# Kernel tuning notes

Measured on AMD Instinct MI355X. Metric: run time of the kernel, lower is better.

Reference implementation:

```python
import jax, jax.numpy as jnp
import numpy as np

N_NODES = 100000
N_EDGES = 1600000
IN_C = 128
HID_C = 16
HEADS = 4
OUT_C = 32
NEG_SLOPE = 0.2


def _gat_conv(x, src, dst, W, a_src, a_dst, b, heads, C):
    """One PyG-style GATConv (v1) with self-loops already appended to src/dst."""
    N = x.shape[0]
    h = (x @ W).reshape(N, heads, C)                      # [N,H,C]
    al_src = jnp.einsum('nhc,hc->nh', h, a_src)           # [N,H]
    al_dst = jnp.einsum('nhc,hc->nh', h, a_dst)           # [N,H]
    e = jax.nn.leaky_relu(al_src[src] + al_dst[dst], NEG_SLOPE)  # [E,H]
    # segment softmax over destination nodes (numerically stable)
    m = jax.ops.segment_max(e, dst, num_segments=N)       # [N,H]
    m = jnp.where(jnp.isfinite(m), m, 0.0)
    ee = jnp.exp(e - m[dst])
    denom = jax.ops.segment_sum(ee, dst, num_segments=N)  # [N,H]
    alpha = ee / denom[dst]                               # [E,H]
    out = jax.ops.segment_sum(h[src] * alpha[:, :, None], dst, num_segments=N)  # [N,H,C]
    return out.reshape(N, heads * C) + b


def setup_inputs() -> dict:
    key = jax.random.key(0)
    ks = jax.random.split(key, 16)
    s = 0.05
    x = jax.random.normal(ks[0], (N_NODES, IN_C), dtype=jnp.float32)
    edge_index = jax.random.randint(ks[1], (2, N_EDGES), 0, N_NODES, dtype=jnp.int64)
    d = {
        'x': x,
        'edge_index': edge_index,
        'W1': jax.random.normal(ks[2], (IN_C, HEADS * HID_C), dtype=jnp.float32) * s,
        'a_src1': jax.random.normal(ks[3], (HEADS, HID_C), dtype=jnp.float32) * s,
        'a_dst1': jax.random.normal(ks[4], (HEADS, HID_C), dtype=jnp.float32) * s,
        'b1': jnp.zeros((HEADS * HID_C,), dtype=jnp.float32),
        'W2': jax.random.normal(ks[5], (HEADS * HID_C, HEADS * HID_C), dtype=jnp.float32) * s,
        'a_src2': jax.random.normal(ks[6], (HEADS, HID_C), dtype=jnp.float32) * s,
        'a_dst2': jax.random.normal(ks[7], (HEADS, HID_C), dtype=jnp.float32) * s,
        'b2': jnp.zeros((HEADS * HID_C,), dtype=jnp.float32),
        'W3': jax.random.normal(ks[8], (HEADS * HID_C, OUT_C), dtype=jnp.float32) * s,
        'a_src3': jax.random.normal(ks[9], (1, OUT_C), dtype=jnp.float32) * s,
        'a_dst3': jax.random.normal(ks[10], (1, OUT_C), dtype=jnp.float32) * s,
        'b3': jnp.zeros((OUT_C,), dtype=jnp.float32),
    }
    return d


def reference(x, edge_index, W1, a_src1, a_dst1, b1, W2, a_src2, a_dst2, b2,
              W3, a_src3, a_dst3, b3):
    N = x.shape[0]
    loop = jnp.arange(N, dtype=edge_index.dtype)
    src = jnp.concatenate([edge_index[0], loop])  # PyG add_self_loops=True
    dst = jnp.concatenate([edge_index[1], loop])
    h = jax.nn.relu(_gat_conv(x, src, dst, W1, a_src1, a_dst1, b1, HEADS, HID_C))
    # dropout p=0.5 is identity in eval mode
    h = jax.nn.relu(_gat_conv(h, src, dst, W2, a_src2, a_dst2, b2, HEADS, HID_C))
    out = _gat_conv(h, src, dst, W3, a_src3, a_dst3, b3, 1, OUT_C)  # [N, OUT_C]
    return out  # .squeeze(-2) is a no-op on [N, OUT_C] with N>1
```

## Files before the change

### kernel.cpp

```cpp
#include <hip/hip_runtime.h>
#include <hip/hip_fp16.h>

#define N_NODES 100000
#define N_EDGES 1600000
#define NPART   8
#define PART_SZ (N_NODES / NPART)
#define CAP 48
#define BSH  10
#define NBIN 98
#define SCAP2 4096
#define SSH2 12
#define EPB  2048

static __device__ __forceinline__ float lrelu(float z) { return z > 0.f ? z : 0.2f * z; }
static __device__ __forceinline__ int imin(int a, int b) { return a < b ? a : b; }

static __device__ __forceinline__ unsigned pack2h(float a, float b) {
    return __builtin_bit_cast(unsigned, __floats2half2_rn(a, b));
}

__global__ __launch_bounds__(256) void bucket_build(const int* __restrict__ ei, int* __restrict__ tails,
                                                    unsigned* __restrict__ stage) {
    __shared__ int lcnt[NBIN];
    __shared__ int lbase[NBIN];
    int tid = threadIdx.x;
    if (tid < NBIN) lcnt[tid] = 0;
    __syncthreads();

    int stripe = blockIdx.x & 7;
    int e0 = blockIdx.x * EPB;
    int binv[EPB / 256];
    int slotv[EPB / 256];
    unsigned vv[EPB / 256];
#pragma unroll
    for (int k = 0; k < EPB / 256; ++k) {
        int t = e0 + k * 256 + tid;
        binv[k] = -1;
        if (t < N_EDGES) {
            int d = __builtin_nontemporal_load(ei + N_EDGES + t);
            int s = __builtin_nontemporal_load(ei + t);
            int b = d >> BSH;
            vv[k] = ((unsigned)(d & ((1 << BSH) - 1)) << 17) | (unsigned)s;
            slotv[k] = atomicAdd(&lcnt[b], 1);
            binv[k] = b;
        }
    }
    __syncthreads();

    if (tid < NBIN) lbase[tid] = atomicAdd(&tails[stripe * 128 + tid], lcnt[tid]);
    __syncthreads();

#pragma unroll
    for (int k = 0; k < EPB / 256; ++k) {
        if (binv[k] >= 0) {
            int pos = lbase[binv[k]] + slotv[k];
            if (pos < SCAP2)
                stage[((((unsigned)binv[k] << 3) | (unsigned)stripe) << SSH2) + (unsigned)pos] = vv[k];
        }
    }
}

__global__ __launch_bounds__(1024) void bucket_fill(const int* __restrict__ tails, const unsigned* __restrict__ stage,
                                                    int* __restrict__ cnt, int* __restrict__ srcs) {
    __shared__ int lc[1 << BSH];
    int tid = threadIdx.x;
    int bin = blockIdx.x;
    int base = bin << BSH;
    int nn = N_NODES - base; if (nn > (1 << BSH)) nn = 1 << BSH;
    if (tid < nn) {
        lc[tid] = 1;
        srcs[(base + tid) * CAP] = base + tid;
    }
    __syncthreads();

    for (int st = 0; st < 8; ++st) {
        int len = tails[st * 128 + bin];
        if (len > SCAP2) len = SCAP2;
        const unsigned* sl = stage + ((((unsigned)bin << 3) | (unsigned)st) << SSH2);
        for (int i = tid; i < len; i += 1024) {
            unsigned v = __builtin_nontemporal_load(sl + i);
            int dloc = (int)(v >> 17);
            int s = (int)(v & 0x1FFFFu);
            int slot = atomicAdd(&lc[dloc], 1);
            if (slot < CAP) srcs[(base + dloc) * CAP + slot] = s;
        }
    }
    __syncthreads();
    if (tid < nn) cnt[base + tid] = lc[tid];
}

template <int IN, int OUT, int HEADS, int NPB>
__global__ __launch_bounds__(256) void gemm_al(const float* __restrict__ x, const float* __restrict__ W,
                                               const float* __restrict__ asrc, const float* __restrict__ adst,
                                               unsigned short* __restrict__ h, float* __restrict__ als,
                                               float* __restrict__ ald) {
    constexpr int SPLIT = OUT / 16;
    constexpr int STRIDE = IN + 1;
    constexpr int F4PT = NPB * (IN / 4) / 256;
    constexpr int KCH = (IN * OUT * 4 > 16384) ? (IN / 2) : IN;
    __shared__ float sx[NPB * STRIDE];
    __shared__ float sw[KCH * OUT];
    int t = threadIdx.x;
    long base = (long)blockIdx.x * NPB;

#pragma unroll
    for (int p = 0; p < F4PT; ++p) {
        int e = p * 256 + t;
        int row = e / (IN / 4);
        int c4 = e % (IN / 4);
        long gr = base + row;
        if (gr >= N_NODES) gr = N_NODES - 1;
        float4 v = *reinterpret_cast<const float4*>(&x[gr * IN + c4 * 4]);
        float* d = &sx[row * STRIDE + c4 * 4];
        d[0] = v.x; d[1] = v.y; d[2] = v.z; d[3] = v.w;
    }

    int w = t >> 6, lane = t & 63;
    int s = __builtin_amdgcn_readfirstlane(w % SPLIT);
    int grp = __builtin_amdgcn_readfirstlane(w / SPLIT);
    int r = grp * 64 + lane;
    long n = base + r;

    float acc[16];
#pragma unroll
    for (int j = 0; j < 16; ++j) acc[j] = 0.f;

    for (int k0 = 0; k0 < IN; k0 += KCH) {
        __syncthreads();
#pragma unroll
        for (int e = t; e < KCH * OUT / 4; e += 256)
            reinterpret_cast<float4*>(sw)[e] =
                reinterpret_cast<const float4*>(W + (long)k0 * OUT)[e];
        __syncthreads();

        const float* swb = sw + s * 16;
#pragma unroll 8
        for (int k = 0; k < KCH; ++k) {
            float xv = sx[r * STRIDE + k0 + k];
            const float* Wr = swb + k * OUT;
#pragma unroll
            for (int j = 0; j < 16; ++j) acc[j] = fmaf(xv, Wr[j], acc[j]);
        }
    }

    if (n < N_NODES) {
        unsigned u[8];
#pragma unroll
        for (int k = 0; k < 8; ++k)
            u[k] = pack2h(acc[2 * k], acc[2 * k + 1]);
        uint4* dst = reinterpret_cast<uint4*>(&h[n * OUT + s * 16]);
        dst[0] = make_uint4(u[0], u[1], u[2], u[3]);
        dst[1] = make_uint4(u[4], u[5], u[6], u[7]);
    }

    float ps = 0.f, pd = 0.f;
#pragma unroll
    for (int j = 0; j < 16; ++j) {
        ps = fmaf(acc[j], asrc[s * 16 + j], ps);
        pd = fmaf(acc[j], adst[s * 16 + j], pd);
    }
    if (HEADS == SPLIT) {
        if (n < N_NODES) {
            als[n * HEADS + s] = ps;
            ald[n * HEADS + s] = pd;
        }
    } else {
        __syncthreads();
        sx[r * 2 + s] = ps;
        sx[NPB * 2 + r * 2 + s] = pd;
        __syncthreads();
        if (t < NPB) {
            long nn = base + t;
            if (nn < N_NODES) {
                als[nn] = sx[t * 2] + sx[t * 2 + 1];
                ald[nn] = sx[NPB * 2 + t * 2] + sx[NPB * 2 + t * 2 + 1];
            }
        }
    }
}

static __device__ __forceinline__ int agg_node(int blk, int wid) {
    return (blk & 7) * PART_SZ + (blk >> 3) * 4 + wid;
}

__global__ __launch_bounds__(256, 8) void agg_h4(const int* __restrict__ cnt, const int* __restrict__ srcs,
                                                 const unsigned short* __restrict__ h, const float* __restrict__ als,
                                                 const float* __restrict__ ald, const float* __restrict__ bias,
                                                 float* __restrict__ g, int do_relu) {
    const uint4* hrow = reinterpret_cast<const uint4*>(h);
    int wid = threadIdx.x >> 6, lane = threadIdx.x & 63;
    int n = agg_node(blockIdx.x, wid);
    if (n >= N_NODES) return;
    int q = lane >> 3, cc = lane & 7;
    int hd = cc >> 1;
    float ad = ald[n * 4 + hd];
    int deg = cnt[n]; if (deg > CAP) deg = CAP;
    int dm1 = deg - 1;
    int sl = srcs[n * CAP + imin(lane, dm1)];

    int s0 = __shfl(sl, imin(0 * 8 + q, dm1));
    int s1 = __shfl(sl, imin(1 * 8 + q, dm1));
    int s2 = __shfl(sl, imin(2 * 8 + q, dm1));
    int s3 = __shfl(sl, imin(3 * 8 + q, dm1));
    float al0 = als[s0 * 4 + hd];
    float al1 = als[s1 * 4 + hd];
    float al2 = als[s2 * 4 + hd];
    float al3 = als[s3 * 4 + hd];
    uint4 hv0 = hrow[(long)s0 * 8 + cc];
    uint4 hv1 = hrow[(long)s1 * 8 + cc];
    uint4 hv2 = hrow[(long)s2 * 8 + cc];
    uint4 hv3 = hrow[(long)s3 * 8 + cc];
    __builtin_amdgcn_sched_barrier(0);

    float a0 = 0.f, a1 = 0.f, a2 = 0.f, a3 = 0.f, a4 = 0.f, a5 = 0.f, a6 = 0.f, a7 = 0.f;
    float den = 0.f;
#define ACCUM(AL, HV, T)                                                \
    {                                                                   \
        float w = ((T) * 8 + q) < deg ? __expf(lrelu((AL) + ad)) : 0.f; \
        den += w;                                                       \
        __half2 p0 = __builtin_bit_cast(__half2, (HV).x);               \
        __half2 p1 = __builtin_bit_cast(__half2, (HV).y);               \
        __half2 p2 = __builtin_bit_cast(__half2, (HV).z);               \
        __half2 p3 = __builtin_bit_cast(__half2, (HV).w);               \
        a0 = fmaf(w, (float)p0.x, a0); a1 = fmaf(w, (float)p0.y, a1);   \
        a2 = fmaf(w, (float)p1.x, a2); a3 = fmaf(w, (float)p1.y, a3);   \
        a4 = fmaf(w, (float)p2.x, a4); a5 = fmaf(w, (float)p2.y, a5);   \
        a6 = fmaf(w, (float)p3.x, a6); a7 = fmaf(w, (float)p3.y, a7);   \
    }
    ACCUM(al0, hv0, 0)
    ACCUM(al1, hv1, 1)
    ACCUM(al2, hv2, 2)
    ACCUM(al3, hv3, 3)

    if (__builtin_expect(deg > 32, 0)) {
        for (int e = 32; e < deg; e += 8) {
            int ee = e + q;
            int s = __shfl(sl, imin(ee, dm1));
            float al = als[s * 4 + hd];
            uint4 hv = hrow[(long)s * 8 + cc];
            float w = ee < deg ? __expf(lrelu(al + ad)) : 0.f;
            den += w;
            __half2 p0 = __builtin_bit_cast(__half2, hv.x);
            __half2 p1 = __builtin_bit_cast(__half2, hv.y);
            __half2 p2 = __builtin_bit_cast(__half2, hv.z);
            __half2 p3 = __builtin_bit_cast(__half2, hv.w);
            a0 = fmaf(w, (float)p0.x, a0); a1 = fmaf(w, (float)p0.y, a1);
            a2 = fmaf(w, (float)p1.x, a2); a3 = fmaf(w, (float)p1.y, a3);
            a4 = fmaf(w, (float)p2.x, a4); a5 = fmaf(w, (float)p2.y, a5);
            a6 = fmaf(w, (float)p3.x, a6); a7 = fmaf(w, (float)p3.y, a7);
        }
    }
#undef ACCUM

#pragma unroll
    for (int d = 8; d <= 32; d <<= 1) {
        a0 += __shfl_xor(a0, d); a1 += __shfl_xor(a1, d);
        a2 += __shfl_xor(a2, d); a3 += __shfl_xor(a3, d);
        a4 += __shfl_xor(a4, d); a5 += __shfl_xor(a5, d);
        a6 += __shfl_xor(a6, d); a7 += __shfl_xor(a7, d);
        den += __shfl_xor(den, d);
    }
    if (q == 0) {
        float4 b0 = *reinterpret_cast<const float4*>(&bias[cc * 8]);
        float4 b1 = *reinterpret_cast<const float4*>(&bias[cc * 8 + 4]);
        float inv = 1.f / den;
        float4 o0, o1;
        o0.x = fmaf(a0, inv, b0.x); o0.y = fmaf(a1, inv, b0.y);
        o0.z = fmaf(a2, inv, b0.z); o0.w = fmaf(a3, inv, b0.w);
        o1.x = fmaf(a4, inv, b1.x); o1.y = fmaf(a5, inv, b1.y);
        o1.z = fmaf(a6, inv, b1.z); o1.w = fmaf(a7, inv, b1.w);
        if (do_relu) {
            o0.x = fmaxf(o0.x, 0.f); o0.y = fmaxf(o0.y, 0.f);
            o0.z = fmaxf(o0.z, 0.f); o0.w = fmaxf(o0.w, 0.f);
            o1.x = fmaxf(o1.x, 0.f); o1.y = fmaxf(o1.y, 0.f);
            o1.z = fmaxf(o1.z, 0.f); o1.w = fmaxf(o1.w, 0.f);
        }
        *reinterpret_cast<float4*>(&g[(long)n * 64 + cc * 8]) = o0;
        *reinterpret_cast<float4*>(&g[(long)n * 64 + cc * 8 + 4]) = o1;
    }
}

__global__ __launch_bounds__(256, 8) void agg_h1(const int* __restrict__ cnt, const int* __restrict__ srcs,
                                                 const unsigned short* __restrict__ h3, const float* __restrict__ als,
                                                 const float* __restrict__ ald, const float* __restrict__ bias,
                                                 float* __restrict__ out) {
    const uint4* hrow = reinterpret_cast<const uint4*>(h3);
    int wid = threadIdx.x >> 6, lane = threadIdx.x & 63;
    int n = agg_node(blockIdx.x, wid);
    if (n >= N_NODES) return;
    int q = lane >> 2, cc = lane & 3;
    float ad = ald[n];
    int deg = cnt[n]; if (deg > CAP) deg = CAP;
    int dm1 = deg - 1;
    int sl = srcs[n * CAP + imin(lane, dm1)];

    int s0 = __shfl(sl, imin(0 * 16 + q, dm1));
    int s1 = __shfl(sl, imin(1 * 16 + q, dm1));
    float al0 = als[s0];
    float al1 = als[s1];
    uint4 hv0 = hrow[(long)s0 * 4 + cc];
    uint4 hv1 = hrow[(long)s1 * 4 + cc];
    __builtin_amdgcn_sched_barrier(0);

    float a0 = 0.f, a1 = 0.f, a2 = 0.f, a3 = 0.f, a4 = 0.f, a5 = 0.f, a6 = 0.f, a7 = 0.f;
    float den = 0.f;
#define ACCUM1(AL, HV, T)                                                \
    {                                                                    \
        float w = ((T) * 16 + q) < deg ? __expf(lrelu((AL) + ad)) : 0.f; \
        den += w;                                                        \
        __half2 p0 = __builtin_bit_cast(__half2, (HV).x);                \
        __half2 p1 = __builtin_bit_cast(__half2, (HV).y);                \
        __half2 p2 = __builtin_bit_cast(__half2, (HV).z);                \
        __half2 p3 = __builtin_bit_cast(__half2, (HV).w);                \
        a0 = fmaf(w, (float)p0.x, a0); a1 = fmaf(w, (float)p0.y, a1);    \
        a2 = fmaf(w, (float)p1.x, a2); a3 = fmaf(w, (float)p1.y, a3);    \
        a4 = fmaf(w, (float)p2.x, a4); a5 = fmaf(w, (float)p2.y, a5);    \
        a6 = fmaf(w, (float)p3.x, a6); a7 = fmaf(w, (float)p3.y, a7);    \
    }
    ACCUM1(al0, hv0, 0)
    ACCUM1(al1, hv1, 1)

    if (__builtin_expect(deg > 32, 0)) {
        for (int e = 32; e < deg; e += 16) {
            int ee = e + q;
            int s = __shfl(sl, imin(ee, dm1));
            float al = als[s];
            uint4 hv = hrow[(long)s * 4 + cc];
            float w = ee < deg ? __expf(lrelu(al + ad)) : 0.f;
            den += w;
            __half2 p0 = __builtin_bit_cast(__half2, hv.x);
            __half2 p1 = __builtin_bit_cast(__half2, hv.y);
            __half2 p2 = __builtin_bit_cast(__half2, hv.z);
            __half2 p3 = __builtin_bit_cast(__half2, hv.w);
            a0 = fmaf(w, (float)p0.x, a0); a1 = fmaf(w, (float)p0.y, a1);
            a2 = fmaf(w, (float)p1.x, a2); a3 = fmaf(w, (float)p1.y, a3);
            a4 = fmaf(w, (float)p2.x, a4); a5 = fmaf(w, (float)p2.y, a5);
            a6 = fmaf(w, (float)p3.x, a6); a7 = fmaf(w, (float)p3.y, a7);
        }
    }
#undef ACCUM1

#pragma unroll
    for (int d = 4; d <= 32; d <<= 1) {
        a0 += __shfl_xor(a0, d); a1 += __shfl_xor(a1, d);
        a2 += __shfl_xor(a2, d); a3 += __shfl_xor(a3, d);
        a4 += __shfl_xor(a4, d); a5 += __shfl_xor(a5, d);
        a6 += __shfl_xor(a6, d); a7 += __shfl_xor(a7, d);
        den += __shfl_xor(den, d);
    }
    if (q == 0) {
        float4 b0 = *reinterpret_cast<const float4*>(&bias[cc * 8]);
        float4 b1 = *reinterpret_cast<const float4*>(&bias[cc * 8 + 4]);
        float inv = 1.f / den;
        float4 o0, o1;
        o0.x = fmaf(a0, inv, b0.x); o0.y = fmaf(a1, inv, b0.y);
        o0.z = fmaf(a2, inv, b0.z); o0.w = fmaf(a3, inv, b0.w);
        o1.x = fmaf(a4, inv, b1.x); o1.y = fmaf(a5, inv, b1.y);
        o1.z = fmaf(a6, inv, b1.z); o1.w = fmaf(a7, inv, b1.w);
        *reinterpret_cast<float4*>(&out[(long)n * 32 + cc * 8]) = o0;
        *reinterpret_cast<float4*>(&out[(long)n * 32 + cc * 8 + 4]) = o1;
    }
}

extern "C" void kernel_launch(void* const* d_in, const int* in_sizes, int n_in,
                              void* d_out, int out_size, void* d_ws, size_t ws_size,
                              hipStream_t stream) {
    (void)in_sizes; (void)n_in; (void)out_size; (void)ws_size;
    const float* x   = (const float*)d_in[0];
    const int*   ei  = (const int*)d_in[1];
    const float* W1  = (const float*)d_in[2];
    const float* as1 = (const float*)d_in[3];
    const float* ad1 = (const float*)d_in[4];
    const float* b1  = (const float*)d_in[5];
    const float* W2  = (const float*)d_in[6];
    const float* as2 = (const float*)d_in[7];
    const float* ad2 = (const float*)d_in[8];
    const float* b2  = (const float*)d_in[9];
    const float* W3  = (const float*)d_in[10];
    const float* as3 = (const float*)d_in[11];
    const float* ad3 = (const float*)d_in[12];
    const float* b3  = (const float*)d_in[13];
    float* out = (float*)d_out;

    char* w = (char*)d_ws;
    auto alloc = [&](size_t bytes) {
        void* p = (void*)w;
        w += (bytes + 255) & ~(size_t)255;
        return p;
    };
    int*            cnt   = (int*)alloc((size_t)N_NODES * 4);
    int*            tails = (int*)alloc((size_t)1024 * 4);
    int*            srcs  = (int*)alloc((size_t)N_NODES * CAP * 4);
    unsigned short* h     = (unsigned short*)alloc((size_t)N_NODES * 64 * 2);
    float*          g     = (float*)alloc((size_t)N_NODES * 64 * 4);
    float*          als   = (float*)alloc((size_t)N_NODES * 4 * 4);
    float*          ald   = (float*)alloc((size_t)N_NODES * 4 * 4);
    unsigned*       stage = (unsigned*)g;

    hipMemsetAsync(tails, 0, (size_t)1024 * 4, stream);

    int g64  = (N_NODES + 63) / 64;
    int g128 = (N_NODES + 127) / 128;
    int gAgg = ((N_NODES + 3) / 4 + 7) & ~7;
    int gBuild = (N_EDGES + EPB - 1) / EPB;

    bucket_build<<<gBuild, 256, 0, stream>>>(ei, tails, stage);
    bucket_fill<<<NBIN, 1024, 0, stream>>>(tails, stage, cnt, srcs);

    gemm_al<128, 64, 4, 64><<<g64, 256, 0, stream>>>(x, W1, as1, ad1, h, als, ald);
    agg_h4<<<gAgg, 256, 0, stream>>>(cnt, srcs, h, als, ald, b1, g, 1);
    gemm_al<64, 64, 4, 64><<<g64, 256, 0, stream>>>(g, W2, as2, ad2, h, als, ald);
    agg_h4<<<gAgg, 256, 0, stream>>>(cnt, srcs, h, als, ald, b2, g, 1);
    gemm_al<64, 32, 1, 128><<<g128, 256, 0, stream>>>(g, W3, as3, ad3, h, als, ald);
    agg_h1<<<gAgg, 256, 0, stream>>>(cnt, srcs, h, als, ald, b3, out);
}
```

Baseline: 355.1 us.

## Compute two rows per thread in gemm_al and stream x in K-chunks

Each thread in the node-feature GEMM now accumulates two node rows, so every weight value loaded from shared memory is reused for two FMAs. The block covers twice as many nodes. The x tile is now loaded per 32-wide K chunk together with the weight chunk instead of all at once, which keeps shared memory bounded. Register pressure doubles for the accumulators, and the grid halves, which may lower occupancy and parallelism.

```diff
diff --git a/kernel.cpp b/kernel.cpp
--- a/kernel.cpp
+++ b/kernel.cpp
@@ -89,45 +89,42 @@
     if (tid < nn) cnt[base + tid] = lc[tid];
 }
 
-template <int IN, int OUT, int HEADS, int NPB>
+template <int IN, int OUT, int HEADS>
 __global__ __launch_bounds__(256) void gemm_al(const float* __restrict__ x, const float* __restrict__ W,
                                                const float* __restrict__ asrc, const float* __restrict__ adst,
                                                unsigned short* __restrict__ h, float* __restrict__ als,
                                                float* __restrict__ ald) {
     constexpr int SPLIT = OUT / 16;
-    constexpr int STRIDE = IN + 1;
-    constexpr int F4PT = NPB * (IN / 4) / 256;
-    constexpr int KCH = (IN * OUT * 4 > 16384) ? (IN / 2) : IN;
-    __shared__ float sx[NPB * STRIDE];
-    __shared__ float sw[KCH * OUT];
+    constexpr int GRP = 4 / SPLIT;
+    constexpr int NPB = 128 * GRP;
+    constexpr int KCH = 32;
+    constexpr int KST = KCH + 1;
+    __shared__ alignas(16) float sx[NPB * KST];
+    __shared__ alignas(16) float sw[KCH * OUT];
     int t = threadIdx.x;
     long base = (long)blockIdx.x * NPB;
 
-#pragma unroll
-    for (int p = 0; p < F4PT; ++p) {
-        int e = p * 256 + t;
-        int row = e / (IN / 4);
-        int c4 = e % (IN / 4);
-        long gr = base + row;
-        if (gr >= N_NODES) gr = N_NODES - 1;
-        float4 v = *reinterpret_cast<const float4*>(&x[gr * IN + c4 * 4]);
-        float* d = &sx[row * STRIDE + c4 * 4];
-        d[0] = v.x; d[1] = v.y; d[2] = v.z; d[3] = v.w;
-    }
-
     int w = t >> 6, lane = t & 63;
     int s = __builtin_amdgcn_readfirstlane(w % SPLIT);
-    int grp = __builtin_amdgcn_readfirstlane(w / SPLIT);
-    int r = grp * 64 + lane;
-    long n = base + r;
-
-    float acc[16];
-#pragma unroll
-    for (int j = 0; j < 16; ++j) acc[j] = 0.f;
+    int rg = __builtin_amdgcn_readfirstlane(w / SPLIT);
+    int r0 = rg * 128 + lane;
+    int r1 = r0 + 64;
+    long n0 = base + r0, n1 = base + r1;
+
+    float acc0[16], acc1[16];
+#pragma unroll
+    for (int j = 0; j < 16; ++j) { acc0[j] = 0.f; acc1[j] = 0.f; }
 
     for (int k0 = 0; k0 < IN; k0 += KCH) {
         __syncthreads();
-#pragma unroll
+        for (int e = t; e < NPB * (KCH / 4); e += 256) {
+            int row = e >> 3, c4 = e & 7;
+            long gr = base + row;
+            if (gr >= N_NODES) gr = N_NODES - 1;
+            float4 v = *reinterpret_cast<const float4*>(&x[gr * IN + k0 + c4 * 4]);
+            float* d = &sx[row * KST + c4 * 4];
+            d[0] = v.x; d[1] = v.y; d[2] = v.z; d[3] = v.w;
+        }
         for (int e = t; e < KCH * OUT / 4; e += 256)
             reinterpret_cast<float4*>(sw)[e] =
                 reinterpret_cast<const float4*>(W + (long)k0 * OUT)[e];
@@ -136,38 +133,49 @@
         const float* swb = sw + s * 16;
 #pragma unroll 8
         for (int k = 0; k < KCH; ++k) {
-            float xv = sx[r * STRIDE + k0 + k];
+            float xv0 = sx[r0 * KST + k];
+            float xv1 = sx[r1 * KST + k];
             const float* Wr = swb + k * OUT;
 #pragma unroll
-            for (int j = 0; j < 16; ++j) acc[j] = fmaf(xv, Wr[j], acc[j]);
-        }
-    }
-
-    if (n < N_NODES) {
+            for (int j = 0; j < 16; ++j) {
+                float wv = Wr[j];
+                acc0[j] = fmaf(xv0, wv, acc0[j]);
+                acc1[j] = fmaf(xv1, wv, acc1[j]);
+            }
+        }
+    }
+
+    if (n0 < N_NODES) {
         unsigned u[8];
 #pragma unroll
-        for (int k = 0; k < 8; ++k)
-            u[k] = pack2h(acc[2 * k], acc[2 * k + 1]);
-        uint4* dst = reinterpret_cast<uint4*>(&h[n * OUT + s * 16]);
+        for (int k = 0; k < 8; ++k) u[k] = pack2h(acc0[2 * k], acc0[2 * k + 1]);
+        uint4* dst = reinterpret_cast<uint4*>(&h[n0 * OUT + s * 16]);
         dst[0] = make_uint4(u[0], u[1], u[2], u[3]);
         dst[1] = make_uint4(u[4], u[5], u[6], u[7]);
     }
-
-    float ps = 0.f, pd = 0.f;
+    if (n1 < N_NODES) {
+        unsigned u[8];
+#pragma unroll
+        for (int k = 0; k < 8; ++k) u[k] = pack2h(acc1[2 * k], acc1[2 * k + 1]);
+        uint4* dst = reinterpret_cast<uint4*>(&h[n1 * OUT + s * 16]);
+        dst[0] = make_uint4(u[0], u[1], u[2], u[3]);
+        dst[1] = make_uint4(u[4], u[5], u[6], u[7]);
+    }
+
+    float ps0 = 0.f, pd0 = 0.f, ps1 = 0.f, pd1 = 0.f;
 #pragma unroll
     for (int j = 0; j < 16; ++j) {
-        ps = fmaf(acc[j], asrc[s * 16 + j], ps);
-        pd = fmaf(acc[j], adst[s * 16 + j], pd);
+        float as = asrc[s * 16 + j], ad = adst[s * 16 + j];
+        ps0 = fmaf(acc0[j], as, ps0); pd0 = fmaf(acc0[j], ad, pd0);
+        ps1 = fmaf(acc1[j], as, ps1); pd1 = fmaf(acc1[j], ad, pd1);
     }
     if (HEADS == SPLIT) {
-        if (n < N_NODES) {
-            als[n * HEADS + s] = ps;
-            ald[n * HEADS + s] = pd;
-        }
+        if (n0 < N_NODES) { als[n0 * HEADS + s] = ps0; ald[n0 * HEADS + s] = pd0; }
+        if (n1 < N_NODES) { als[n1 * HEADS + s] = ps1; ald[n1 * HEADS + s] = pd1; }
     } else {
         __syncthreads();
-        sx[r * 2 + s] = ps;
-        sx[NPB * 2 + r * 2 + s] = pd;
+        sx[r0 * 2 + s] = ps0;            sx[r1 * 2 + s] = ps1;
+        sx[NPB * 2 + r0 * 2 + s] = pd0;  sx[NPB * 2 + r1 * 2 + s] = pd1;
         __syncthreads();
         if (t < NPB) {
             long nn = base + t;
@@ -273,7 +281,7 @@
             o0.x = fmaxf(o0.x, 0.f); o0.y = fmaxf(o0.y, 0.f);
             o0.z = fmaxf(o0.z, 0.f); o0.w = fmaxf(o0.w, 0.f);
             o1.x = fmaxf(o1.x, 0.f); o1.y = fmaxf(o1.y, 0.f);
-            o1.z = fmaxf(o1.z, 0.f); o1.w = fmaxf(o1.w, 0.f);
+            o1.w = fmaxf(o1.w, 0.f); o1.z = fmaxf(o1.z, 0.f);
         }
         *reinterpret_cast<float4*>(&g[(long)n * 64 + cc * 8]) = o0;
         *reinterpret_cast<float4*>(&g[(long)n * 64 + cc * 8 + 4]) = o1;
@@ -399,18 +407,18 @@
 
     hipMemsetAsync(tails, 0, (size_t)1024 * 4, stream);
 
-    int g64  = (N_NODES + 63) / 64;
     int g128 = (N_NODES + 127) / 128;
+    int g256 = (N_NODES + 255) / 256;
     int gAgg = ((N_NODES + 3) / 4 + 7) & ~7;
     int gBuild = (N_EDGES + EPB - 1) / EPB;
 
     bucket_build<<<gBuild, 256, 0, stream>>>(ei, tails, stage);
     bucket_fill<<<NBIN, 1024, 0, stream>>>(tails, stage, cnt, srcs);
 
-    gemm_al<128, 64, 4, 64><<<g64, 256, 0, stream>>>(x, W1, as1, ad1, h, als, ald);
+    gemm_al<128, 64, 4><<<g128, 256, 0, stream>>>(x, W1, as1, ad1, h, als, ald);
     agg_h4<<<gAgg, 256, 0, stream>>>(cnt, srcs, h, als, ald, b1, g, 1);
-    gemm_al<64, 64, 4, 64><<<g64, 256, 0, stream>>>(g, W2, as2, ad2, h, als, ald);
+    gemm_al<64, 64, 4><<<g128, 256, 0, stream>>>(g, W2, as2, ad2, h, als, ald);
     agg_h4<<<gAgg, 256, 0, stream>>>(cnt, srcs, h, als, ald, b2, g, 1);
-    gemm_al<64, 32, 1, 128><<<g128, 256, 0, stream>>>(g, W3, as3, ad3, h, als, ald);
+    gemm_al<64, 32, 1><<<g256, 256, 0, stream>>>(g, W3, as3, ad3, h, als, ald);
     agg_h1<<<gAgg, 256, 0, stream>>>(cnt, srcs, h, als, ald, b3, out);
 }
```

New measurement: 359.7 us. Within noise of the previous version (+1.3%).
